# Kernel optimization log

Measured on AMD Instinct MI355X. Metric: run time of the kernel, lower is better.

## Reference

```python
import jax, jax.numpy as jnp
import numpy as np

# dims
T, INPUT_DIM = 128, 512
C_INT, ISQ, DIM, C = 8, 16, 256, 8  # internal_channels, input_square_dim, dim, n_channel
OSQ, OUT_CH = 8, 16                  # output_square_dim, output_size // osq^2
INPUT_SCALE, S1, S2 = 1.0, 0.9, 0.1
K1, D1, K2, D2 = 3, 1, 5, 2


def dw_circ_conv(x, w, dilation):
    """Depthwise conv with circular padding. x: [B,C,H,W], w: [C,1,k,k]."""
    k = w.shape[-1]
    pad = dilation * (k - 1) // 2
    xp = jnp.pad(x, ((0, 0), (0, 0), (pad, pad), (pad, pad)), mode='wrap')
    return jax.lax.conv_general_dilated(
        xp, w, window_strides=(1, 1), padding='VALID',
        rhs_dilation=(dilation, dilation), feature_group_count=x.shape[1])


def setup_inputs() -> dict:
    key = jax.random.key(0)
    ks = jax.random.split(key, 10)
    X = jax.random.normal(ks[0], (T, INPUT_DIM), jnp.float32)
    # nn.Linear weight [out, in]
    W_embed = jax.random.normal(ks[1], (C_INT * ISQ * ISQ, INPUT_DIM), jnp.float32) * 0.02
    mask_coarse = jax.random.bernoulli(ks[2], 0.5, (1, 1, ISQ, ISQ)).astype(jnp.float32)
    mask_fine = jax.random.bernoulli(ks[3], 0.5, (1, 1, DIM, DIM)).astype(jnp.float32)
    # ConvTranspose2d weight [in_ch, out_ch, k, k], k = dim // isq = 16
    W_deconv = jax.random.normal(ks[4], (C_INT, C, DIM // ISQ, DIM // ISQ), jnp.float32) * 0.02

    def lateral_w(k, ksz, p):
        # LateralConnections with conn_exp=1: |w| * bernoulli(p), normalized per output channel
        w = jnp.abs(jax.random.normal(k, (C, 1, ksz, ksz), jnp.float32))
        m = jax.random.bernoulli(jax.random.fold_in(k, 1), p, w.shape).astype(jnp.float32)
        w = w * m
        return w / w.sum(axis=(1, 2, 3), keepdims=True)

    w1 = lateral_w(ks[5], K1, 0.9)
    w2 = lateral_w(ks[6], K2, 0.9)
    # output Conv2d: [out_ch, in_ch, k, k], k = dim // osq = 32
    w_out = jax.random.normal(ks[7], (OUT_CH, C, DIM // OSQ, DIM // OSQ), jnp.float32) * 0.01
    b_out = jax.random.normal(ks[8], (OUT_CH,), jnp.float32) * 0.01
    return dict(X=X, W_embed=W_embed, mask_coarse=mask_coarse, mask_fine=mask_fine,
                W_deconv=W_deconv, w1=w1, w2=w2, w_out=w_out, b_out=b_out)


def reference(X, W_embed, mask_coarse, mask_fine, W_deconv, w1, w2, w_out, b_out):
    t = X.shape[0]
    ksz = W_deconv.shape[-1]
    # CorticalInput
    u = (X @ W_embed.T).reshape(t, C_INT, ISQ, ISQ) * mask_coarse  # [T,Cint,isq,isq]
    # ConvTranspose2d with stride == kernel_size (non-overlapping) == block expansion
    u = jnp.einsum('tcij,coab->toiajb', u, W_deconv).reshape(t, C, ISQ * ksz, ISQ * ksz)
    u = INPUT_SCALE * u * mask_fine  # [T,C,dim,dim]

    # sequential reservoir scan
    def step(Z, x):
        Z = jnp.tanh(S1 * dw_circ_conv(Z, w1, D1) + S2 * dw_circ_conv(Z, w2, D2) + x)
        return Z, Z[0]

    Z0 = jnp.zeros((1, C, DIM, DIM), X.dtype)
    _, outs = jax.lax.scan(step, Z0, u)  # outs: [T,C,dim,dim]

    # readout conv (kernel == stride == dim // osq)
    ko = w_out.shape[-1]
    y = jax.lax.conv_general_dilated(outs, w_out, (ko, ko), 'VALID')
    y = y + b_out[None, :, None, None]
    return y.reshape(t, -1)
```

## Files before the change

### kernel.cpp

```cpp
#include <hip/hip_runtime.h>
#include <math.h>

#define SB_OFF   0
#define E_OFF    1048576

__device__ __forceinline__ float fast_tanh(float x) {
  x = fminf(fmaxf(x, -15.f), 15.f);
  float ex = __expf(2.f * x);
  return __fdividef(ex - 1.f, ex + 1.f);
}

template <int CTRL>
__device__ __forceinline__ float dpp_add(float v) {
  int x = __builtin_amdgcn_update_dpp(0, __float_as_int(v), CTRL, 0xF, 0xF, true);
  return v + __int_as_float(x);
}

__device__ __forceinline__ float2 aload_f2(const float* p) {
  unsigned long long v = __hip_atomic_load((const unsigned long long*)p,
                                           __ATOMIC_RELAXED, __HIP_MEMORY_SCOPE_AGENT);
  float2 r;
  r.x = __uint_as_float((unsigned)v);
  r.y = __uint_as_float((unsigned)(v >> 32));
  return r;
}
__device__ __forceinline__ void astore_f2(float* p, float a, float b) {
  unsigned long long v =
      ((unsigned long long)__float_as_uint(b) << 32) | (unsigned long long)__float_as_uint(a);
  __hip_atomic_store((unsigned long long*)p, v, __ATOMIC_RELAXED, __HIP_MEMORY_SCOPE_AGENT);
}

__global__ __launch_bounds__(256) void prep_kernel(
    const float* __restrict__ X, const float* __restrict__ W_embed,
    const float* __restrict__ mask_coarse, const float* __restrict__ b_out,
    float* __restrict__ ws, float* __restrict__ out)
{
  const int tid = threadIdx.x, bid = blockIdx.x;
  float* eb = ws + E_OFF;
  {
    int idx = bid * 256 + tid;
    out[idx] = b_out[(idx >> 6) & 15];
  }
  const int o  = bid * 4 + (tid >> 6);
  const int t0 = (tid & 63) * 2;
  const float4* Wf4 = (const float4*)W_embed + (size_t)o * 128;
  const float4* Xf4 = (const float4*)X;
  float a0 = 0.f, a1 = 0.f;
  for (int k4 = 0; k4 < 128; ++k4) {
    float4 wv = Wf4[k4];
    float4 x0 = Xf4[(size_t)t0 * 128 + k4];
    float4 x1 = Xf4[(size_t)(t0 + 1) * 128 + k4];
    a0 = fmaf(wv.x, x0.x, fmaf(wv.y, x0.y, fmaf(wv.z, x0.z, fmaf(wv.w, x0.w, a0))));
    a1 = fmaf(wv.x, x1.x, fmaf(wv.y, x1.y, fmaf(wv.z, x1.z, fmaf(wv.w, x1.w, a1))));
  }
  float mc = mask_coarse[o & 255];
  eb[(size_t)t0 * 2048 + o]       = a0 * mc;
  eb[(size_t)(t0 + 1) * 2048 + o] = a1 * mc;
}

__global__ __launch_bounds__(512, 2) void scan_kernel(
    const float* __restrict__ mask_fine, const float* __restrict__ W_deconv,
    const float* __restrict__ w1, const float* __restrict__ w2,
    const float* __restrict__ w_out, float* __restrict__ ws,
    float* __restrict__ out)
{
  __shared__ float zin[2][72 * 44];
  __shared__ float rowbuf[2][64 * 17];

  const int tid  = threadIdx.x;
  const int bid  = blockIdx.x;
  const int ch   = bid >> 5;
  const int tile = bid & 31;
  const int tI = tile >> 3, tJ = tile & 7;
  const int r0 = tI << 6, c0 = tJ << 5;
  const int row = tid >> 3;
  const int cg  = tid & 7;
  const int lc  = cg << 2;

  float* Zb = ws + SB_OFF;
  const float* eb = ws + E_OFF;
  const int myoff = (ch * 32 + tile) << 11;

  const int i0 = (r0 + row) >> 4;
  const int jj = (c0 + lc) >> 4;
  float4 wd[8];
#pragma unroll
  for (int c = 0; c < 8; ++c)
    wd[c] = *(const float4*)&W_deconv[(((c * 8 + ch) * 16) + (row & 15)) * 16 + (lc & 15)];
  float4 mf = *(const float4*)&mask_fine[(size_t)(r0 + row) * 256 + c0 + lc];
  float4 wo[16];
#pragma unroll
  for (int oc = 0; oc < 16; ++oc)
    wo[oc] = *(const float4*)&w_out[(((oc * 8 + ch) * 32) + (row & 31)) * 32 + lc];
  float w1s[9], w2s[25];
#pragma unroll
  for (int k = 0; k < 9; ++k)
    w1s[k] = __uint_as_float(__builtin_amdgcn_readfirstlane(__float_as_uint(w1[ch * 9 + k])));
#pragma unroll
  for (int k = 0; k < 25; ++k)
    w2s[k] = __uint_as_float(__builtin_amdgcn_readfirstlane(__float_as_uint(w2[ch * 25 + k])));

  int rd_off[2] = {0, 0}, rd_dst[2] = {0, 0};
  {
    int n = 0;
    auto setup = [&](int u) {
      int di = 0, dj = 0, off = 0, dst = 0;
      if (u < 128) {
        int r = u >> 5, c = u & 31;
        di = -1; dj = 0; off = 256 + 2 * u; dst = r * 44 + 4 + c;
      } else if (u < 256) {
        int v = u - 128;
        di = 1; dj = 0; off = 2 * v; dst = (68 + (v >> 5)) * 44 + 4 + (v & 31);
      } else if (u < 512) {
        int v = u - 256;
        di = 0; dj = -1; off = 1024 + 2 * v; dst = (4 + (v >> 2)) * 44 + (v & 3);
      } else if (u < 768) {
        int v = u - 512;
        di = 0; dj = 1; off = 512 + 2 * v; dst = (4 + (v >> 2)) * 44 + 36 + (v & 3);
      } else {
        int v = u - 768; int corner = v >> 4, k = v & 15, r = k >> 2, c = k & 3;
        if (corner == 0)      { di = -1; dj = -1; off = 1632 + 2 * k; dst = r * 44 + c; }
        else if (corner == 1) { di = -1; dj = 1;  off = 1600 + 2 * k; dst = r * 44 + 36 + c; }
        else if (corner == 2) { di = 1;  dj = -1; off = 1568 + 2 * k; dst = (68 + r) * 44 + c; }
        else                  { di = 1;  dj = 1;  off = 1536 + 2 * k; dst = (68 + r) * 44 + 36 + c; }
      }
      int nI = (tI + di) & 3, nJ = (tJ + dj) & 7;
      rd_off[n] = ((ch * 32 + nI * 8 + nJ) << 11) + off;
      rd_dst[n] = dst;
      ++n;
    };
    setup(tid);
    if (tid < 320) setup(tid + 512);
  }
  const bool has2 = (tid < 320);

  for (int k = tid; k < 2 * 72 * 44; k += 512) zin[0][k] = 0.f;
  __syncthreads();

  for (int t = 0; t < 128; ++t) {
    float* sb = Zb + (size_t)((t + 1) & 1) * 524288;
    const float* zr = zin[t & 1];
    float*       zw = zin[(t + 1) & 1];
    float*       rb = rowbuf[t & 1];

    float ev[8];
#pragma unroll
    for (int c = 0; c < 8; ++c)
      ev[c] = eb[(size_t)t * 2048 + c * 256 + i0 * 16 + jj];

    float c1a[4] = {0, 0, 0, 0}, c2a[4] = {0, 0, 0, 0};
    {
      float w[12];
      auto load_row = [&](int zrr) {
        float4 A  = *(const float4*)&zr[zrr * 44 + lc];
        float4 B  = *(const float4*)&zr[zrr * 44 + lc + 4];
        float4 Cq = *(const float4*)&zr[zrr * 44 + lc + 8];
        w[0]=A.x; w[1]=A.y; w[2]=A.z; w[3]=A.w;
        w[4]=B.x; w[5]=B.y; w[6]=B.z; w[7]=B.w;
        w[8]=Cq.x; w[9]=Cq.y; w[10]=Cq.z; w[11]=Cq.w;
      };
      auto k2row = [&](int a) {
#pragma unroll
        for (int j = 0; j < 4; ++j)
#pragma unroll
          for (int b = 0; b < 5; ++b)
            c2a[j] = fmaf(w[j + 2 * b], w2s[a * 5 + b], c2a[j]);
      };
      auto k1row = [&](int a) {
#pragma unroll
        for (int j = 0; j < 4; ++j)
#pragma unroll
          for (int b = 0; b < 3; ++b)
            c1a[j] = fmaf(w[j + 3 + b], w1s[a * 3 + b], c1a[j]);
      };
      load_row(row + 0); k2row(0);
      load_row(row + 2); k2row(1);
      load_row(row + 3); k1row(0);
      load_row(row + 4); k1row(1); k2row(2);
      load_row(row + 5); k1row(2);
      load_row(row + 6); k2row(3);
      load_row(row + 8); k2row(4);
    }
    float zv[4];
    {
      const float* mfp = (const float*)&mf;
#pragma unroll
      for (int j = 0; j < 4; ++j) {
        float u = 0.f;
#pragma unroll
        for (int c = 0; c < 8; ++c)
          u = fmaf(ev[c], ((const float*)&wd[c])[j], u);
        float val = fmaf(0.9f, c1a[j], fmaf(0.1f, c2a[j], mfp[j] * u));
        zv[j] = fast_tanh(val);
      }
    }

    if (t < 127) {
      float* myrec = sb + myoff;
      const float tagf = __uint_as_float((unsigned)(t + 1));
      if (row < 4) {
#pragma unroll
        for (int j = 0; j < 4; ++j)
          astore_f2(myrec + 2 * (row * 32 + lc + j), zv[j], tagf);
      }
      if (row >= 60) {
#pragma unroll
        for (int j = 0; j < 4; ++j)
          astore_f2(myrec + 256 + 2 * ((row - 60) * 32 + lc + j), zv[j], tagf);
      }
      if (lc == 0) {
#pragma unroll
        for (int j = 0; j < 4; ++j)
          astore_f2(myrec + 512 + 2 * (row * 4 + j), zv[j], tagf);
      }
      if (lc == 28) {
#pragma unroll
        for (int j = 0; j < 4; ++j)
          astore_f2(myrec + 1024 + 2 * (row * 4 + j), zv[j], tagf);
      }
      if (row < 4 && lc == 0) {
#pragma unroll
        for (int j = 0; j < 4; ++j)
          astore_f2(myrec + 1536 + 2 * (row * 4 + j), zv[j], tagf);
      }
      if (row < 4 && lc == 28) {
#pragma unroll
        for (int j = 0; j < 4; ++j)
          astore_f2(myrec + 1568 + 2 * (row * 4 + j), zv[j], tagf);
      }
      if (row >= 60 && lc == 0) {
#pragma unroll
        for (int j = 0; j < 4; ++j)
          astore_f2(myrec + 1600 + 2 * ((row - 60) * 4 + j), zv[j], tagf);
      }
      if (row >= 60 && lc == 28) {
#pragma unroll
        for (int j = 0; j < 4; ++j)
          astore_f2(myrec + 1632 + 2 * ((row - 60) * 4 + j), zv[j], tagf);
      }
    }

    *(float4*)&zw[(4 + row) * 44 + 4 + lc] = make_float4(zv[0], zv[1], zv[2], zv[3]);

    float racc[16];
#pragma unroll
    for (int oc = 0; oc < 16; ++oc) {
      const float* wop = (const float*)&wo[oc];
      racc[oc] = fmaf(zv[0], wop[0], fmaf(zv[1], wop[1], fmaf(zv[2], wop[2], zv[3] * wop[3])));
    }
#pragma unroll
    for (int k = 0; k < 16; ++k) {
      racc[k] = dpp_add<0xB1>(racc[k]);
      racc[k] = dpp_add<0x4E>(racc[k]);
      racc[k] = dpp_add<0x141>(racc[k]);
    }
    rb[row * 17 + (cg << 1)]     = racc[cg << 1];
    rb[row * 17 + (cg << 1) + 1] = racc[(cg << 1) + 1];

    if (t < 127) {
      const unsigned tg = (unsigned)(t + 1);
      const float* p0 = sb + rd_off[0];
      const float* p1 = sb + rd_off[has2 ? 1 : 0];
      float2 va = aload_f2(p0);
      float2 vb = aload_f2(p1);
      int spins = 0;
      while ((__float_as_uint(va.y) != tg) || (__float_as_uint(vb.y) != tg)) {
        if (++spins > (1 << 18)) break;
        __builtin_amdgcn_s_sleep(1);
        if (__float_as_uint(va.y) != tg) va = aload_f2(p0);
        if (__float_as_uint(vb.y) != tg) vb = aload_f2(p1);
      }
      zw[rd_dst[0]] = va.x;
      if (has2) zw[rd_dst[1]] = vb.x;
    }

    __syncthreads();

    if (tid < 32) {
      int p = tid >> 4, oc = tid & 15;
      float s = 0.f;
#pragma unroll
      for (int r = 0; r < 32; ++r) s += rb[(p * 32 + r) * 17 + oc];
      atomicAdd(&out[t * 1024 + oc * 64 + (2 * tI + p) * 8 + tJ], s);
    }
  }
}

extern "C" void kernel_launch(void* const* d_in, const int* in_sizes, int n_in,
                              void* d_out, int out_size, void* d_ws, size_t ws_size,
                              hipStream_t stream) {
  const float* X           = (const float*)d_in[0];
  const float* W_embed     = (const float*)d_in[1];
  const float* mask_coarse = (const float*)d_in[2];
  const float* mask_fine   = (const float*)d_in[3];
  const float* W_deconv    = (const float*)d_in[4];
  const float* w1          = (const float*)d_in[5];
  const float* w2          = (const float*)d_in[6];
  const float* w_out       = (const float*)d_in[7];
  const float* b_out       = (const float*)d_in[8];
  float* ws  = (float*)d_ws;
  float* out = (float*)d_out;

  prep_kernel<<<dim3(512), dim3(256), 0, stream>>>(X, W_embed, mask_coarse, b_out, ws, out);
  scan_kernel<<<dim3(256), dim3(512), 0, stream>>>(mask_fine, W_deconv, w1, w2, w_out, ws, out);
}
```

Before: 573.7 us.

## Replace per-value tagged halo exchange with packed float4 data plus per-wave tags

Halo values exchanged between tile blocks each step were stored as interleaved (value, tag) 64-bit atomics. They are now written as packed float4 records with cache-bypass stores. Each wavefront then publishes one tag after waiting for its stores to drain. Readers spin on a single per-wave tag, then load 16 bytes of data, which halves the exchange footprint and cuts the number of readers from 832 to 208 threads. The cost is a store-drain wait before each tag, inline asm with sc0/sc1 cache bits, and correctness that depends on memory ordering between the data stores and the tag.

```diff
diff --git a/kernel.cpp b/kernel.cpp
--- a/kernel.cpp
+++ b/kernel.cpp
@@ -2,7 +2,9 @@
 #include <math.h>
 
 #define SB_OFF   0
-#define E_OFF    1048576
+#define E_OFF    524288
+
+typedef float vf4 __attribute__((ext_vector_type(4)));
 
 __device__ __forceinline__ float fast_tanh(float x) {
   x = fminf(fmaxf(x, -15.f), 15.f);
@@ -16,18 +18,20 @@
   return v + __int_as_float(x);
 }
 
-__device__ __forceinline__ float2 aload_f2(const float* p) {
-  unsigned long long v = __hip_atomic_load((const unsigned long long*)p,
-                                           __ATOMIC_RELAXED, __HIP_MEMORY_SCOPE_AGENT);
-  float2 r;
-  r.x = __uint_as_float((unsigned)v);
-  r.y = __uint_as_float((unsigned)(v >> 32));
+__device__ __forceinline__ void st16(float* p, float a, float b, float c, float d) {
+  vf4 v; v.x = a; v.y = b; v.z = c; v.w = d;
+  asm volatile("global_store_dwordx4 %0, %1, off sc0 sc1" :: "v"(p), "v"(v) : "memory");
+}
+__device__ __forceinline__ vf4 ld16(const float* p) {
+  vf4 r;
+  asm volatile("global_load_dwordx4 %0, %1, off sc0 sc1\n"
+               "s_waitcnt vmcnt(0)"
+               : "=&v"(r) : "v"(p) : "memory");
   return r;
 }
-__device__ __forceinline__ void astore_f2(float* p, float a, float b) {
-  unsigned long long v =
-      ((unsigned long long)__float_as_uint(b) << 32) | (unsigned long long)__float_as_uint(a);
-  __hip_atomic_store((unsigned long long*)p, v, __ATOMIC_RELAXED, __HIP_MEMORY_SCOPE_AGENT);
+__device__ __forceinline__ void tag_store(unsigned* p, unsigned v) {
+  asm volatile("s_waitcnt vmcnt(0)\n"
+               "global_store_dword %0, %1, off sc0 sc1" :: "v"(p), "v"(v) : "memory");
 }
 
 __global__ __launch_bounds__(256) void prep_kernel(
@@ -79,7 +83,7 @@
 
   float* Zb = ws + SB_OFF;
   const float* eb = ws + E_OFF;
-  const int myoff = (ch * 32 + tile) << 11;
+  const int myoff = (ch * 32 + tile) << 10;
 
   const int i0 = (r0 + row) >> 4;
   const int jj = (c0 + lc) >> 4;
@@ -100,45 +104,39 @@
   for (int k = 0; k < 25; ++k)
     w2s[k] = __uint_as_float(__builtin_amdgcn_readfirstlane(__float_as_uint(w2[ch * 25 + k])));
 
-  int rd_off[2] = {0, 0}, rd_dst[2] = {0, 0};
-  {
-    int n = 0;
-    auto setup = [&](int u) {
-      int di = 0, dj = 0, off = 0, dst = 0;
-      if (u < 128) {
-        int r = u >> 5, c = u & 31;
-        di = -1; dj = 0; off = 256 + 2 * u; dst = r * 44 + 4 + c;
-      } else if (u < 256) {
-        int v = u - 128;
-        di = 1; dj = 0; off = 2 * v; dst = (68 + (v >> 5)) * 44 + 4 + (v & 31);
-      } else if (u < 512) {
-        int v = u - 256;
-        di = 0; dj = -1; off = 1024 + 2 * v; dst = (4 + (v >> 2)) * 44 + (v & 3);
-      } else if (u < 768) {
-        int v = u - 512;
-        di = 0; dj = 1; off = 512 + 2 * v; dst = (4 + (v >> 2)) * 44 + 36 + (v & 3);
-      } else {
-        int v = u - 768; int corner = v >> 4, k = v & 15, r = k >> 2, c = k & 3;
-        if (corner == 0)      { di = -1; dj = -1; off = 1632 + 2 * k; dst = r * 44 + c; }
-        else if (corner == 1) { di = -1; dj = 1;  off = 1600 + 2 * k; dst = r * 44 + 36 + c; }
-        else if (corner == 2) { di = 1;  dj = -1; off = 1568 + 2 * k; dst = (68 + r) * 44 + c; }
-        else                  { di = 1;  dj = 1;  off = 1536 + 2 * k; dst = (68 + r) * 44 + 36 + c; }
-      }
-      int nI = (tI + di) & 3, nJ = (tJ + dj) & 7;
-      rd_off[n] = ((ch * 32 + nI * 8 + nJ) << 11) + off;
-      rd_dst[n] = dst;
-      ++n;
-    };
-    setup(tid);
-    if (tid < 320) setup(tid + 512);
-  }
-  const bool has2 = (tid < 320);
+  int rd_src = 0, rd_dst = 0, rd_tag = 0;
+  const bool hasrd = (tid < 208);
+  if (hasrd) {
+    int u = tid, di = 0, dj = 0, src = 0, dst = 0, wv = 0;
+    if (u < 32) {
+      di = -1; src = 128 + (u >> 3) * 32 + (u & 7) * 4;
+      dst = (u >> 3) * 44 + 4 + (u & 7) * 4; wv = 7;
+    } else if (u < 64) {
+      int v = u - 32; di = 1; src = (v >> 3) * 32 + (v & 7) * 4;
+      dst = (68 + (v >> 3)) * 44 + 4 + (v & 7) * 4; wv = 0;
+    } else if (u < 128) {
+      int v = u - 64; dj = -1; src = 512 + v * 4; dst = (4 + v) * 44; wv = v >> 3;
+    } else if (u < 192) {
+      int v = u - 128; dj = 1; src = 256 + v * 4; dst = (4 + v) * 44 + 36; wv = v >> 3;
+    } else {
+      int v = u - 192, c = v >> 2, r = v & 3;
+      if (c == 0)      { di = -1; dj = -1; src = 816 + r * 4; dst = r * 44;            wv = 7; }
+      else if (c == 1) { di = -1; dj = 1;  src = 800 + r * 4; dst = r * 44 + 36;       wv = 7; }
+      else if (c == 2) { di = 1;  dj = -1; src = 784 + r * 4; dst = (68 + r) * 44;     wv = 0; }
+      else             { di = 1;  dj = 1;  src = 768 + r * 4; dst = (68 + r) * 44 + 36; wv = 0; }
+    }
+    int nI = (tI + di) & 3, nJ = (tJ + dj) & 7;
+    int roff = (ch * 32 + nI * 8 + nJ) << 10;
+    rd_src = roff + src;
+    rd_tag = roff + 832 + wv * 16;
+    rd_dst = dst;
+  }
 
   for (int k = tid; k < 2 * 72 * 44; k += 512) zin[0][k] = 0.f;
   __syncthreads();
 
   for (int t = 0; t < 128; ++t) {
-    float* sb = Zb + (size_t)((t + 1) & 1) * 524288;
+    float* sb = Zb + (size_t)((t + 1) & 1) * 262144;
     const float* zr = zin[t & 1];
     float*       zw = zin[(t + 1) & 1];
     float*       rb = rowbuf[t & 1];
@@ -196,48 +194,17 @@
     }
 
     if (t < 127) {
-      float* myrec = sb + myoff;
-      const float tagf = __uint_as_float((unsigned)(t + 1));
-      if (row < 4) {
-#pragma unroll
-        for (int j = 0; j < 4; ++j)
-          astore_f2(myrec + 2 * (row * 32 + lc + j), zv[j], tagf);
-      }
-      if (row >= 60) {
-#pragma unroll
-        for (int j = 0; j < 4; ++j)
-          astore_f2(myrec + 256 + 2 * ((row - 60) * 32 + lc + j), zv[j], tagf);
-      }
-      if (lc == 0) {
-#pragma unroll
-        for (int j = 0; j < 4; ++j)
-          astore_f2(myrec + 512 + 2 * (row * 4 + j), zv[j], tagf);
-      }
-      if (lc == 28) {
-#pragma unroll
-        for (int j = 0; j < 4; ++j)
-          astore_f2(myrec + 1024 + 2 * (row * 4 + j), zv[j], tagf);
-      }
-      if (row < 4 && lc == 0) {
-#pragma unroll
-        for (int j = 0; j < 4; ++j)
-          astore_f2(myrec + 1536 + 2 * (row * 4 + j), zv[j], tagf);
-      }
-      if (row < 4 && lc == 28) {
-#pragma unroll
-        for (int j = 0; j < 4; ++j)
-          astore_f2(myrec + 1568 + 2 * (row * 4 + j), zv[j], tagf);
-      }
-      if (row >= 60 && lc == 0) {
-#pragma unroll
-        for (int j = 0; j < 4; ++j)
-          astore_f2(myrec + 1600 + 2 * ((row - 60) * 4 + j), zv[j], tagf);
-      }
-      if (row >= 60 && lc == 28) {
-#pragma unroll
-        for (int j = 0; j < 4; ++j)
-          astore_f2(myrec + 1632 + 2 * ((row - 60) * 4 + j), zv[j], tagf);
-      }
+      float* rec = sb + myoff;
+      if (row < 4)   st16(rec + row * 32 + lc, zv[0], zv[1], zv[2], zv[3]);
+      if (row >= 60) st16(rec + 128 + (row - 60) * 32 + lc, zv[0], zv[1], zv[2], zv[3]);
+      if (lc == 0)   st16(rec + 256 + row * 4, zv[0], zv[1], zv[2], zv[3]);
+      if (lc == 28)  st16(rec + 512 + row * 4, zv[0], zv[1], zv[2], zv[3]);
+      if (row < 4 && lc == 0)   st16(rec + 768 + row * 4, zv[0], zv[1], zv[2], zv[3]);
+      if (row < 4 && lc == 28)  st16(rec + 784 + row * 4, zv[0], zv[1], zv[2], zv[3]);
+      if (row >= 60 && lc == 0) st16(rec + 800 + (row - 60) * 4, zv[0], zv[1], zv[2], zv[3]);
+      if (row >= 60 && lc == 28) st16(rec + 816 + (row - 60) * 4, zv[0], zv[1], zv[2], zv[3]);
+      if ((tid & 63) == 0)
+        tag_store((unsigned*)(rec + 832 + (tid >> 6) * 16), (unsigned)(t + 1));
     }
 
     *(float4*)&zw[(4 + row) * 44 + 4 + lc] = make_float4(zv[0], zv[1], zv[2], zv[3]);
@@ -257,21 +224,19 @@
     rb[row * 17 + (cg << 1)]     = racc[cg << 1];
     rb[row * 17 + (cg << 1) + 1] = racc[(cg << 1) + 1];
 
-    if (t < 127) {
+    if (t < 127 && hasrd) {
       const unsigned tg = (unsigned)(t + 1);
-      const float* p0 = sb + rd_off[0];
-      const float* p1 = sb + rd_off[has2 ? 1 : 0];
-      float2 va = aload_f2(p0);
-      float2 vb = aload_f2(p1);
+      const unsigned* ta = (const unsigned*)(sb + rd_tag);
       int spins = 0;
-      while ((__float_as_uint(va.y) != tg) || (__float_as_uint(vb.y) != tg)) {
+      while (__hip_atomic_load(ta, __ATOMIC_RELAXED, __HIP_MEMORY_SCOPE_AGENT) != tg) {
+        __builtin_amdgcn_s_sleep(1);
         if (++spins > (1 << 18)) break;
-        __builtin_amdgcn_s_sleep(1);
-        if (__float_as_uint(va.y) != tg) va = aload_f2(p0);
-        if (__float_as_uint(vb.y) != tg) vb = aload_f2(p1);
       }
-      zw[rd_dst[0]] = va.x;
-      if (has2) zw[rd_dst[1]] = vb.x;
+      vf4 v = ld16(sb + rd_src);
+      zw[rd_dst]     = v.x;
+      zw[rd_dst + 1] = v.y;
+      zw[rd_dst + 2] = v.z;
+      zw[rd_dst + 3] = v.w;
     }
 
     __syncthreads();
```

After: 556.1 us. 3.1% less time.
